# Performance work log

Hardware: AMD Instinct MI355X
Metric: run time of the kernel (lower is better)

The kernel has to match this reference:

```python
import jax, jax.numpy as jnp
import numpy as np

D = 1024
H = 16
DK = D // H  # 64
CHUNK = 64
EPS = 1e-5


def setup_inputs() -> dict:
    key = jax.random.key(0)
    k1, k2, k3 = jax.random.split(key, 3)
    x = jax.random.normal(k1, (4, 4096, D), dtype=jnp.float32)
    W_qkv = jax.random.normal(k2, (D, 3 * D), dtype=jnp.float32) * 0.02
    W_o = jax.random.normal(k3, (D, D), dtype=jnp.float32) * 0.02
    return {"x": x, "W_qkv": W_qkv, "W_o": W_o}


def _layernorm_noaffine(k):
    mu = jnp.mean(k, axis=-1, keepdims=True)
    var = jnp.mean((k - mu) ** 2, axis=-1, keepdims=True)  # biased var, torch LayerNorm
    return (k - mu) / jnp.sqrt(var + EPS)


def _linear_attn(x, W_qkv, W_o):
    B, L, Dm = x.shape
    qkv = (x @ W_qkv).reshape(B, L, 3, H, DK)
    q, k, v = qkv[:, :, 0], qkv[:, :, 1], qkv[:, :, 2]
    k = _layernorm_noaffine(k)

    nC = L // CHUNK
    # [nC, B, C, H, DK] for scan over chunks
    to_chunks = lambda t: t.reshape(B, nC, CHUNK, H, DK).transpose(1, 0, 2, 3, 4)
    qc, kc, vc = to_chunks(q), to_chunks(k), to_chunks(v)

    causal = jnp.tril(jnp.ones((CHUNK, CHUNK), dtype=bool))  # s <= t inclusive

    def step(S, chunk):
        q_c, k_c, v_c = chunk  # each [B, C, H, DK]
        # inter-chunk: y_t += S_prev @ q_t
        inter = jnp.einsum('bhde,bthe->bthd', S, q_c)
        # intra-chunk: y_t += sum_{s<=t} (k_s . q_t) v_s
        scores = jnp.einsum('bthd,bshd->bhts', q_c, k_c)
        scores = jnp.where(causal, scores, 0.0)
        intra = jnp.einsum('bhts,bshd->bthd', scores, v_c)
        # state update: S += sum_t v_t k_t^T
        S = S + jnp.einsum('bthd,bthe->bhde', v_c, k_c)
        return S, inter + intra

    S0 = jnp.zeros((B, H, DK, DK), dtype=x.dtype)
    _, ys = jax.lax.scan(step, S0, (qc, kc, vc))  # ys: [nC, B, C, H, DK]
    y = ys.transpose(1, 0, 2, 3, 4).reshape(B, L, Dm)
    return y @ W_o


def reference(x, W_qkv, W_o):
    return _linear_attn(x, W_qkv, W_o)
```

## Files before the change

kernel.cpp:

```cpp
#include <hip/hip_runtime.h>

#define EPS 1e-5f

typedef __attribute__((ext_vector_type(8))) short s16x8;
typedef __attribute__((ext_vector_type(4))) float f4;

__device__ __forceinline__ short f2bf(float f) {
  union { float f; unsigned u; } x; x.f = f;
  unsigned r = x.u + 0x7fffu + ((x.u >> 16) & 1u);
  return (short)(r >> 16);
}
__device__ __forceinline__ float bf2f(short s) {
  union { unsigned u; float f; } x; x.u = ((unsigned)(unsigned short)s) << 16;
  return x.f;
}
__device__ __forceinline__ void gll16(const short* g, short* l) {
  __builtin_amdgcn_global_load_lds((const __attribute__((address_space(1))) void*)g,
                                   (__attribute__((address_space(3))) void*)l, 16, 0, 0);
}

#define BAR() asm volatile("s_barrier" ::: "memory")
#define LGKM0() do { asm volatile("s_waitcnt lgkmcnt(0)" ::: "memory"); \
                     __builtin_amdgcn_sched_barrier(0); } while (0)

__global__ __launch_bounds__(256) void prep(
    const float* __restrict__ x, const float* __restrict__ Wqkv,
    const float* __restrict__ Wo,
    short* __restrict__ xb, short* __restrict__ WqkvT, short* __restrict__ WoT)
{
  __shared__ float tile[32][33];
  const int bid = blockIdx.x;
  if (bid < 8192) {
    const size_t i = ((size_t)bid * 256 + threadIdx.x) * 8;
    const float4* p = reinterpret_cast<const float4*>(x + i);
    float4 a = p[0], b = p[1];
    union { uint4 v; short s[8]; } o;
    o.s[0] = f2bf(a.x); o.s[1] = f2bf(a.y); o.s[2] = f2bf(a.z); o.s[3] = f2bf(a.w);
    o.s[4] = f2bf(b.x); o.s[5] = f2bf(b.y); o.s[6] = f2bf(b.z); o.s[7] = f2bf(b.w);
    *reinterpret_cast<uint4*>(xb + i) = o.v;
    return;
  }
  const float* W; short* WT; int K, N, t;
  if (bid < 11264) { W = Wqkv; WT = WqkvT; K = 1024; N = 3072; t = bid - 8192;  }
  else             { W = Wo;   WT = WoT;   K = 1024; N = 1024; t = bid - 11264; }
  const int nblk = N >> 5;
  const int n0 = (t % nblk) * 32, k0 = (t / nblk) * 32;
  const int tx = threadIdx.x & 31, ty = threadIdx.x >> 5;
  #pragma unroll
  for (int i = 0; i < 4; i++) {
    int r = ty + i * 8;
    tile[r][tx] = W[(size_t)(k0 + r) * N + n0 + tx];
  }
  __syncthreads();
  #pragma unroll
  for (int i = 0; i < 4; i++) {
    int r = ty + i * 8;
    WT[(size_t)(n0 + r) * K + k0 + tx] = f2bf(tile[tx][r]);
  }
}

__device__ __forceinline__ void stage_slice(const short* __restrict__ G, short* dstbase,
                                            int row0, int kcol, int rowgrp, int panel, int lane) {
  short* dst = dstbase + panel * 8192 + rowgrp * 512;
  const short* src = G + (size_t)(row0 + rowgrp * 16 + (lane >> 2)) * 1024
                       + kcol + panel * 32 + (((lane & 3) << 3) ^ ((lane >> 5) << 4));
  gll16(src, dst);
}

template<bool STAGE>
__device__ __forceinline__ void ktile8p(
    const short* ldsAc, const short* ldsBc, short* ldsAn, short* ldsBn,
    const short* __restrict__ A, const short* __restrict__ BT,
    int m0, int n0, int knext,
    int w, int lane, int wm, int wn, int quad, int l16,
    f4 (&acc)[8][4])
{
  s16x8 bfr[4][2];
  const int co = (quad << 3) ^ ((l16 >> 3) << 4);
  #pragma unroll
  for (int p = 0; p < 4; ++p) {
    s16x8 a00, a01, a10, a11;
    {
      const int r0 = (wm * 128 + p * 32 + l16) * 32;
      a00 = *reinterpret_cast<const s16x8*>(&ldsAc[r0 + co]);
      a01 = *reinterpret_cast<const s16x8*>(&ldsAc[8192 + r0 + co]);
      a10 = *reinterpret_cast<const s16x8*>(&ldsAc[r0 + 512 + co]);
      a11 = *reinterpret_cast<const s16x8*>(&ldsAc[8192 + r0 + 512 + co]);
    }
    if (p == 0) {
      #pragma unroll
      for (int nf = 0; nf < 4; ++nf) {
        const int rb = (wn * 64 + nf * 16 + l16) * 32;
        bfr[nf][0] = *reinterpret_cast<const s16x8*>(&ldsBc[rb + co]);
        bfr[nf][1] = *reinterpret_cast<const s16x8*>(&ldsBc[8192 + rb + co]);
      }
    }
    if (STAGE) {
      if (p == 0)      { stage_slice(BT, ldsBn, n0, knext, w,     0, lane); stage_slice(BT, ldsBn, n0, knext, w,     1, lane); }
      else if (p == 1) { stage_slice(BT, ldsBn, n0, knext, 8 + w, 0, lane); stage_slice(BT, ldsBn, n0, knext, 8 + w, 1, lane); }
      else if (p == 2) { const int rg = (w & 3) + ((w >> 2) << 3);
                         stage_slice(A, ldsAn, m0, knext, rg, 0, lane); stage_slice(A, ldsAn, m0, knext, rg, 1, lane); }
      else             { const int rg = 4 + (w & 3) + ((w >> 2) << 3);
                         stage_slice(A, ldsAn, m0, knext, rg, 0, lane); stage_slice(A, ldsAn, m0, knext, rg, 1, lane); }
    }
    BAR();
    LGKM0();
    __builtin_amdgcn_s_setprio(1);
    #pragma unroll
    for (int nf = 0; nf < 4; ++nf) {
      acc[2*p  ][nf] = __builtin_amdgcn_mfma_f32_16x16x32_bf16(a00, bfr[nf][0], acc[2*p  ][nf], 0, 0, 0);
      acc[2*p  ][nf] = __builtin_amdgcn_mfma_f32_16x16x32_bf16(a01, bfr[nf][1], acc[2*p  ][nf], 0, 0, 0);
      acc[2*p+1][nf] = __builtin_amdgcn_mfma_f32_16x16x32_bf16(a10, bfr[nf][0], acc[2*p+1][nf], 0, 0, 0);
      acc[2*p+1][nf] = __builtin_amdgcn_mfma_f32_16x16x32_bf16(a11, bfr[nf][1], acc[2*p+1][nf], 0, 0, 0);
    }
    __builtin_amdgcn_s_setprio(0);
    if (p == 1) {
      if (STAGE) asm volatile("s_waitcnt vmcnt(4)" ::: "memory");
      else       asm volatile("s_waitcnt vmcnt(0)" ::: "memory");
    }
    if (p == 3 && STAGE) asm volatile("s_waitcnt vmcnt(2)" ::: "memory");
    BAR();
  }
}

#define GEMM8P_PROLOGUE()                                                            \
  stage_slice(BT, Bb0, n0, 0, w,     0, lane); stage_slice(BT, Bb0, n0, 0, w,     1, lane); \
  stage_slice(BT, Bb0, n0, 0, 8 + w, 0, lane); stage_slice(BT, Bb0, n0, 0, 8 + w, 1, lane); \
  { const int rg = (w & 3) + ((w >> 2) << 3);                                        \
    stage_slice(A, Ab0, m0, 0, rg, 0, lane); stage_slice(A, Ab0, m0, 0, rg, 1, lane); } \
  { const int rg = 4 + (w & 3) + ((w >> 2) << 3);                                    \
    stage_slice(A, Ab0, m0, 0, rg, 0, lane); stage_slice(A, Ab0, m0, 0, rg, 1, lane); } \
  asm volatile("s_waitcnt vmcnt(2)" ::: "memory");                                   \
  BAR()

#define GEMM8P_MAINLOOP()                                                            \
  _Pragma("unroll 1")                                                                \
  for (int t = 0; t < 14; t += 2) {                                                  \
    ktile8p<true>(Ab0, Bb0, Ab1, Bb1, A, BT, m0, n0, (t + 1) << 6, w, lane, wm, wn, quad, l16, acc); \
    ktile8p<true>(Ab1, Bb1, Ab0, Bb0, A, BT, m0, n0, (t + 2) << 6, w, lane, wm, wn, quad, l16, acc); \
  }                                                                                  \
  ktile8p<true >(Ab0, Bb0, Ab1, Bb1, A, BT, m0, n0, 15 << 6, w, lane, wm, wn, quad, l16, acc); \
  ktile8p<false>(Ab1, Bb1, Ab0, Bb0, A, BT, m0, n0, 0,       w, lane, wm, wn, quad, l16, acc)

__global__ __launch_bounds__(512, 2) void gemm_qkv_8p(
    const short* __restrict__ A, const short* __restrict__ BT,
    short* __restrict__ qb, short* __restrict__ kb, short* __restrict__ vb)
{
  extern __shared__ __align__(16) short lds[];
  short* Ab0 = lds;           short* Ab1 = lds + 16384;
  short* Bb0 = lds + 32768;   short* Bb1 = lds + 49152;

  const int pid = blockIdx.x;
  const int wg = (pid & 7) * 96 + (pid >> 3);
  const int mb = wg / 12, nb = wg % 12;
  const int m0 = mb * 256, n0 = nb * 256;

  const int tid = threadIdx.x;
  const int w = tid >> 6, lane = tid & 63, quad = lane >> 4, l16 = lane & 15;
  const int wm = w >> 2, wn = w & 3;

  f4 acc[8][4];
  #pragma unroll
  for (int i = 0; i < 8; i++)
    #pragma unroll
    for (int j = 0; j < 4; j++) acc[i][j] = {0.f, 0.f, 0.f, 0.f};

  GEMM8P_PROLOGUE();
  GEMM8P_MAINLOOP();

  __syncthreads();
  short* st = lds + w * 1152;
  const int j0 = n0 + wn * 64;
  const int sq = j0 >> 10;
  const int hh = (j0 >> 6) & 15;
  short* dbuf = (sq == 0) ? qb : (sq == 1) ? kb : vb;
  const int r2 = lane >> 3, c8 = (lane & 7) << 3;
  #pragma unroll
  for (int mf = 0; mf < 8; ++mf) {
    #pragma unroll
    for (int nf = 0; nf < 4; ++nf)
      #pragma unroll
      for (int r = 0; r < 4; ++r)
        st[(quad * 4 + r) * 72 + nf * 16 + l16] = f2bf(acc[mf][nf][r]);
    #pragma unroll
    for (int h2 = 0; h2 < 2; ++h2) {
      int rr = h2 * 8 + r2;
      int i = m0 + wm * 128 + mf * 16 + rr;
      int bb = i >> 12, ll = i & 4095;
      uint4 val = *reinterpret_cast<const uint4*>(&st[rr * 72 + c8]);
      *reinterpret_cast<uint4*>(&dbuf[(((size_t)(bb * 16 + hh)) * 4096 + ll) * 64 + c8]) = val;
    }
  }
}

__global__ __launch_bounds__(512, 2) void gemm_out_8p(
    const short* __restrict__ A, const short* __restrict__ BT, float* __restrict__ C)
{
  extern __shared__ __align__(16) short lds[];
  short* Ab0 = lds;           short* Ab1 = lds + 16384;
  short* Bb0 = lds + 32768;   short* Bb1 = lds + 49152;

  const int pid = blockIdx.x;
  const int wg = (pid & 7) * 32 + (pid >> 3);
  const int mb = wg >> 2, nb = wg & 3;
  const int m0 = mb * 256, n0 = nb * 256;

  const int tid = threadIdx.x;
  const int w = tid >> 6, lane = tid & 63, quad = lane >> 4, l16 = lane & 15;
  const int wm = w >> 2, wn = w & 3;

  f4 acc[8][4];
  #pragma unroll
  for (int i = 0; i < 8; i++)
    #pragma unroll
    for (int j = 0; j < 4; j++) acc[i][j] = {0.f, 0.f, 0.f, 0.f};

  GEMM8P_PROLOGUE();
  GEMM8P_MAINLOOP();

  #pragma unroll
  for (int mf = 0; mf < 8; ++mf)
    #pragma unroll
    for (int nf = 0; nf < 4; ++nf)
      #pragma unroll
      for (int r = 0; r < 4; ++r) {
        int i = m0 + wm * 128 + mf * 16 + quad * 4 + r;
        int j = n0 + wn * 64 + nf * 16 + l16;
        C[(size_t)i * 1024 + j] = acc[mf][nf][r];
      }
}

__global__ __launch_bounds__(256) void gemm_qkv_v4(
    const short* __restrict__ A, const short* __restrict__ BT,
    short* __restrict__ qb, short* __restrict__ kb, short* __restrict__ vb)
{
  __shared__ __align__(16) short lds[8192];
  short* As = lds;
  short* Bs = lds + 4096;

  const int p = blockIdx.x;
  const int slot = p >> 3;
  const int strip = (p & 7) + 8 * (slot / 24);
  const int nb = slot % 24;
  const int m0 = strip * 128, n0 = nb * 128;

  const int tid = threadIdx.x;
  const int w = tid >> 6, lane = tid & 63, quad = lane >> 4, l16 = lane & 15;
  const int wm = (w >> 1) << 6, wn = (w & 1) << 6;

  f4 acc[4][4];
  #pragma unroll
  for (int i = 0; i < 4; i++)
    #pragma unroll
    for (int j = 0; j < 4; j++) acc[i][j] = {0.f, 0.f, 0.f, 0.f};

  const int row = w * 32 + (lane >> 2), ofs = (lane & 3) << 3;

  for (int k0 = 0; k0 < 1024; k0 += 32) {
    __syncthreads();
    gll16(A + (size_t)(m0 + row) * 1024 + k0 + ofs, &As[(w * 32) * 32]);
    gll16(A + (size_t)(m0 + row + 16) * 1024 + k0 + ofs, &As[(w * 32 + 16) * 32]);
    gll16(BT + (size_t)(n0 + row) * 1024 + k0 + ofs, &Bs[(w * 32) * 32]);
    gll16(BT + (size_t)(n0 + row + 16) * 1024 + k0 + ofs, &Bs[(w * 32 + 16) * 32]);
    __syncthreads();
    s16x8 afr[4], bfr[4];
    #pragma unroll
    for (int t = 0; t < 4; t++)
      afr[t] = *reinterpret_cast<const s16x8*>(&As[(wm + t * 16 + l16) * 32 + quad * 8]);
    #pragma unroll
    for (int t = 0; t < 4; t++)
      bfr[t] = *reinterpret_cast<const s16x8*>(&Bs[(wn + t * 16 + l16) * 32 + quad * 8]);
    #pragma unroll
    for (int ti = 0; ti < 4; ti++)
      #pragma unroll
      for (int tj = 0; tj < 4; tj++)
        acc[ti][tj] = __builtin_amdgcn_mfma_f32_16x16x32_bf16(afr[ti], bfr[tj], acc[ti][tj], 0, 0, 0);
  }

  __syncthreads();
  short* st = &lds[w * 16 * 72];
  const int j0 = n0 + wn;
  const int sq = j0 >> 10;
  const int hh = (j0 >> 6) & 15;
  short* dbuf = (sq == 0) ? qb : (sq == 1) ? kb : vb;
  const int r2 = lane >> 3, c8 = (lane & 7) << 3;
  #pragma unroll
  for (int ti = 0; ti < 4; ti++) {
    #pragma unroll
    for (int tj = 0; tj < 4; tj++)
      #pragma unroll
      for (int r = 0; r < 4; r++)
        st[(quad * 4 + r) * 72 + tj * 16 + l16] = f2bf(acc[ti][tj][r]);
    #pragma unroll
    for (int h2 = 0; h2 < 2; h2++) {
      int rr = h2 * 8 + r2;
      int i = m0 + wm + ti * 16 + rr;
      int bb = i >> 12, ll = i & 4095;
      uint4 val = *reinterpret_cast<const uint4*>(&st[rr * 72 + c8]);
      *reinterpret_cast<uint4*>(&dbuf[(((size_t)(bb * 16 + hh)) * 4096 + ll) * 64 + c8]) = val;
    }
  }
}

__global__ __launch_bounds__(256) void ln_k(short* __restrict__ kbuf)
{
  const int row = blockIdx.x * 4 + (threadIdx.x >> 6);
  const int lane = threadIdx.x & 63;
  const size_t idx = (size_t)row * 64 + lane;
  float v = bf2f(kbuf[idx]);
  float s = v, s2 = v * v;
  #pragma unroll
  for (int off = 32; off; off >>= 1) {
    s += __shfl_xor(s, off);
    s2 += __shfl_xor(s2, off);
  }
  float mean = s * (1.f / 64.f);
  float var = s2 * (1.f / 64.f) - mean * mean;
  float rstd = rsqrtf(var + EPS);
  kbuf[idx] = f2bf((v - mean) * rstd);
}

__global__ __launch_bounds__(256) void macro_outer(
    const short* __restrict__ kb, const short* __restrict__ vb,
    short* __restrict__ G)
{
  __shared__ __align__(16) short kT[64 * 72];
  __shared__ __align__(16) short vT[64 * 72];
  const int bh = blockIdx.x >> 4, mc = blockIdx.x & 15;
  const int tid = threadIdx.x;
  const int w = tid >> 6, lane = tid & 63, quad = lane >> 4, l16 = lane & 15;
  const int srow = tid >> 2, sseg = (tid & 3) << 4;
  const int toff = ((((srow >> 3) ^ ((tid & 3) << 1)) & 7) << 3) + (srow & 7);
  const int gsw = (w & 3) << 1;

  f4 accG[4];
  #pragma unroll
  for (int tj = 0; tj < 4; tj++) accG[tj] = {0.f, 0.f, 0.f, 0.f};

  for (int j = 0; j < 4; ++j) {
    if (j) __syncthreads();
    const size_t base = (size_t)bh * 262144 + (size_t)((mc * 4 + j) * 64 + srow) * 64 + sseg;
    {
      const float4* kp = reinterpret_cast<const float4*>(kb + base);
      union { float4 v[2]; short s[16]; } ku;
      ku.v[0] = kp[0]; ku.v[1] = kp[1];
      float kv[16]; float s = 0.f, s2 = 0.f;
      #pragma unroll
      for (int i = 0; i < 16; i++) { kv[i] = bf2f(ku.s[i]); s += kv[i]; s2 += kv[i] * kv[i]; }
      s += __shfl_xor(s, 1);  s2 += __shfl_xor(s2, 1);
      s += __shfl_xor(s, 2);  s2 += __shfl_xor(s2, 2);
      float mean = s * (1.f / 64.f);
      float var = s2 * (1.f / 64.f) - mean * mean;
      float rstd = rsqrtf(var + EPS);
      #pragma unroll
      for (int i = 0; i < 16; i++) kT[(sseg + i) * 72 + toff] = f2bf((kv[i] - mean) * rstd);
      const float4* vp = reinterpret_cast<const float4*>(vb + base);
      union { float4 v[2]; short s[16]; } vu;
      vu.v[0] = vp[0]; vu.v[1] = vp[1];
      #pragma unroll
      for (int i = 0; i < 16; i++) vT[(sseg + i) * 72 + toff] = vu.s[i];
    }
    __syncthreads();
    s16x8 va0 = *reinterpret_cast<const s16x8*>(&vT[(w * 16 + l16) * 72 + ((quad ^ gsw) << 3)]);
    s16x8 va1 = *reinterpret_cast<const s16x8*>(&vT[(w * 16 + l16) * 72 + (((4 + quad) ^ gsw) << 3)]);
    #pragma unroll
    for (int tj = 0; tj < 4; tj++) {
      const int gk = tj << 1;
      s16x8 kb0 = *reinterpret_cast<const s16x8*>(&kT[(tj * 16 + l16) * 72 + ((quad ^ gk) << 3)]);
      s16x8 kb1 = *reinterpret_cast<const s16x8*>(&kT[(tj * 16 + l16) * 72 + (((4 + quad) ^ gk) << 3)]);
      accG[tj] = __builtin_amdgcn_mfma_f32_16x16x32_bf16(va0, kb0, accG[tj], 0, 0, 0);
      accG[tj] = __builtin_amdgcn_mfma_f32_16x16x32_bf16(va1, kb1, accG[tj], 0, 0, 0);
    }
  }
  short* Gc = G + (size_t)blockIdx.x * 4096;
  #pragma unroll
  for (int tj = 0; tj < 4; tj++)
    #pragma unroll
    for (int r = 0; r < 4; r++)
      Gc[(w * 16 + quad * 4 + r) * 64 + tj * 16 + l16] = f2bf(accG[tj][r]);
}

__global__ __launch_bounds__(128) void prefix_S16(short* __restrict__ G)
{
  const int bh = blockIdx.x >> 3, rg = blockIdx.x & 7;
  short* p = G + (size_t)bh * 65536 + rg * 512 + threadIdx.x * 4;
  float s0 = 0.f, s1 = 0.f, s2 = 0.f, s3 = 0.f;
  union U { uint2 v; short s[4]; };
  U cur; cur.v = *reinterpret_cast<const uint2*>(p);
  #pragma unroll 4
  for (int mc = 0; mc < 16; mc++) {
    short* pc = p + (size_t)mc * 4096;
    U nxt; nxt.v = cur.v;
    if (mc < 15) nxt.v = *reinterpret_cast<const uint2*>(pc + 4096);
    float g0 = bf2f(cur.s[0]), g1 = bf2f(cur.s[1]), g2 = bf2f(cur.s[2]), g3 = bf2f(cur.s[3]);
    U su;
    su.s[0] = f2bf(s0); su.s[1] = f2bf(s1); su.s[2] = f2bf(s2); su.s[3] = f2bf(s3);
    *reinterpret_cast<uint2*>(pc) = su.v;
    s0 += g0; s1 += g1; s2 += g2; s3 += g3;
    cur = nxt;
  }
}

__global__ __launch_bounds__(256) void macro_out(
    const short* __restrict__ qb, const short* __restrict__ kb,
    const short* __restrict__ vb, const short* __restrict__ G,
    short* __restrict__ yb)
{
  __shared__ __align__(16) short ks[64 * 72];
  __shared__ __align__(16) short kT[64 * 72];
  __shared__ __align__(16) short vT[64 * 72];
  __shared__ __align__(16) short Sb[64 * 72];
  __shared__ __align__(16) short Ps[64 * 72];
  const int bh = blockIdx.x >> 4, mc = blockIdx.x & 15;
  const int b = bh >> 4, h = bh & 15;
  const int tid = threadIdx.x;
  const int w = tid >> 6, lane = tid & 63, quad = lane >> 4, l16 = lane & 15;
  const int srow = tid >> 2, sseg = (tid & 3) << 4;
  const int toff = ((((srow >> 3) ^ ((tid & 3) << 1)) & 7) << 3) + (srow & 7);
  const int gsw = (w & 3) << 1;
  const int rq2 = ((l16 >> 2) & 3) << 1;

  const short* Sg = G + (size_t)blockIdx.x * 4096;
  f4 accS[4];
  #pragma unroll
  for (int tj = 0; tj < 4; tj++)
    #pragma unroll
    for (int r = 0; r < 4; r++)
      accS[tj][r] = bf2f(Sg[(w * 16 + quad * 4 + r) * 64 + tj * 16 + l16]);

  for (int j = 0; j < 4; ++j) {
    const int c = mc * 4 + j;
    if (j) __syncthreads();
    #pragma unroll
    for (int tj = 0; tj < 4; tj++) {
      const int eb = (tj << 1) + (l16 >> 3);
      const int sbc = (((eb ^ (quad << 1)) & 7) << 3) + (l16 & 7);
      #pragma unroll
      for (int r = 0; r < 4; r++)
        Sb[(w * 16 + quad * 4 + r) * 72 + sbc] = f2bf(accS[tj][r]);
    }
    const size_t base = (size_t)bh * 262144 + (size_t)(c * 64 + srow) * 64 + sseg;
    {
      const float4* kp = reinterpret_cast<const float4*>(kb + base);
      union { float4 v[2]; short s[16]; } ku;
      ku.v[0] = kp[0]; ku.v[1] = kp[1];
      float kv[16]; float s = 0.f, s2 = 0.f;
      #pragma unroll
      for (int i = 0; i < 16; i++) { kv[i] = bf2f(ku.s[i]); s += kv[i]; s2 += kv[i] * kv[i]; }
      s += __shfl_xor(s, 1);  s2 += __shfl_xor(s2, 1);
      s += __shfl_xor(s, 2);  s2 += __shfl_xor(s2, 2);
      float mean = s * (1.f / 64.f);
      float var = s2 * (1.f / 64.f) - mean * mean;
      float rstd = rsqrtf(var + EPS);
      union { float4 v[2]; short s[16]; } ko;
      #pragma unroll
      for (int i = 0; i < 16; i++) ko.s[i] = f2bf((kv[i] - mean) * rstd);
      *reinterpret_cast<float4*>(&ks[srow * 72 + sseg]) = ko.v[0];
      *reinterpret_cast<float4*>(&ks[srow * 72 + sseg + 8]) = ko.v[1];
      #pragma unroll
      for (int i = 0; i < 16; i++) kT[(sseg + i) * 72 + toff] = ko.s[i];
      const float4* vp = reinterpret_cast<const float4*>(vb + base);
      union { float4 v[2]; short s[16]; } vu;
      vu.v[0] = vp[0]; vu.v[1] = vp[1];
      #pragma unroll
      for (int i = 0; i < 16; i++) vT[(sseg + i) * 72 + toff] = vu.s[i];
    }
    s16x8 qa[4][2];
    const size_t qbase = (size_t)bh * 262144 + (size_t)c * 4096;
    #pragma unroll
    for (int ti = 0; ti < 4; ti++)
      #pragma unroll
      for (int kh = 0; kh < 2; kh++)
        qa[ti][kh] = *reinterpret_cast<const s16x8*>(
            qb + qbase + (size_t)(ti * 16 + l16) * 64 + kh * 32 + quad * 8);
    __syncthreads();
    s16x8 kf[2], sf[2];
    #pragma unroll
    for (int kh = 0; kh < 2; kh++) {
      kf[kh] = *reinterpret_cast<const s16x8*>(&ks[(w * 16 + l16) * 72 + kh * 32 + quad * 8]);
      sf[kh] = *reinterpret_cast<const s16x8*>(&Sb[(w * 16 + l16) * 72 + ((((kh << 2) + quad) ^ rq2) << 3)]);
    }
    const int psoff = (((((w * 16 + l16) >> 3) ^ (quad << 1)) & 7) << 3) + (l16 & 7);
    #pragma unroll
    for (int ti = 0; ti < 4; ti++) {
      f4 z = {0.f, 0.f, 0.f, 0.f};
      z = __builtin_amdgcn_mfma_f32_16x16x32_bf16(qa[ti][0], kf[0], z, 0, 0, 0);
      z = __builtin_amdgcn_mfma_f32_16x16x32_bf16(qa[ti][1], kf[1], z, 0, 0, 0);
      #pragma unroll
      for (int r = 0; r < 4; r++) {
        int t = ti * 16 + quad * 4 + r;
        int s = w * 16 + l16;
        Ps[t * 72 + psoff] = (s <= t) ? f2bf(z[r]) : (short)0;
      }
    }
    __syncthreads();
    s16x8 vf0 = *reinterpret_cast<const s16x8*>(&vT[(w * 16 + l16) * 72 + ((quad ^ gsw) << 3)]);
    s16x8 vf1 = *reinterpret_cast<const s16x8*>(&vT[(w * 16 + l16) * 72 + (((4 + quad) ^ gsw) << 3)]);
    #pragma unroll
    for (int ti = 0; ti < 4; ti++) {
      f4 z = {0.f, 0.f, 0.f, 0.f};
      s16x8 p0 = *reinterpret_cast<const s16x8*>(&Ps[(ti * 16 + l16) * 72 + ((quad ^ rq2) << 3)]);
      s16x8 p1 = *reinterpret_cast<const s16x8*>(&Ps[(ti * 16 + l16) * 72 + (((4 + quad) ^ rq2) << 3)]);
      z = __builtin_amdgcn_mfma_f32_16x16x32_bf16(p0, vf0, z, 0, 0, 0);
      z = __builtin_amdgcn_mfma_f32_16x16x32_bf16(p1, vf1, z, 0, 0, 0);
      z = __builtin_amdgcn_mfma_f32_16x16x32_bf16(qa[ti][0], sf[0], z, 0, 0, 0);
      z = __builtin_amdgcn_mfma_f32_16x16x32_bf16(qa[ti][1], sf[1], z, 0, 0, 0);
      #pragma unroll
      for (int r = 0; r < 4; r++) {
        int t = ti * 16 + quad * 4 + r;
        int d = w * 16 + l16;
        yb[(((size_t)b * 4096) + c * 64 + t) * 1024 + h * 64 + d] = f2bf(z[r]);
      }
    }
    #pragma unroll
    for (int tj = 0; tj < 4; tj++) {
      const int gk = tj << 1;
      s16x8 ub0 = *reinterpret_cast<const s16x8*>(&kT[(tj * 16 + l16) * 72 + ((quad ^ gk) << 3)]);
      s16x8 ub1 = *reinterpret_cast<const s16x8*>(&kT[(tj * 16 + l16) * 72 + (((4 + quad) ^ gk) << 3)]);
      accS[tj] = __builtin_amdgcn_mfma_f32_16x16x32_bf16(vf0, ub0, accS[tj], 0, 0, 0);
      accS[tj] = __builtin_amdgcn_mfma_f32_16x16x32_bf16(vf1, ub1, accS[tj], 0, 0, 0);
    }
  }
}

__global__ __launch_bounds__(256) void gemm_out_v3(
    const short* __restrict__ A, const short* __restrict__ BT, float* __restrict__ C)
{
  __shared__ __align__(16) short As[128 * 32];
  __shared__ __align__(16) short Bs[128 * 32];
  const int p = blockIdx.x;
  const int slot = p >> 3;
  const int strip = (p & 7) + 8 * (slot >> 3);
  const int nb = slot & 7;
  const int m0 = strip * 128, n0 = nb * 128;
  const int tid = threadIdx.x;
  const int w = tid >> 6, lane = tid & 63, quad = lane >> 4, l16 = lane & 15;
  const int wm = (w >> 1) << 6, wn = (w & 1) << 6;

  f4 acc[4][4];
  #pragma unroll
  for (int i = 0; i < 4; i++)
    #pragma unroll
    for (int j = 0; j < 4; j++) acc[i][j] = {0.f, 0.f, 0.f, 0.f};

  const int row = w * 32 + (lane >> 2), ofs = (lane & 3) << 3;

  for (int k0 = 0; k0 < 1024; k0 += 32) {
    __syncthreads();
    gll16(A + (size_t)(m0 + row) * 1024 + k0 + ofs, &As[(w * 32) * 32]);
    gll16(A + (size_t)(m0 + row + 16) * 1024 + k0 + ofs, &As[(w * 32 + 16) * 32]);
    gll16(BT + (size_t)(n0 + row) * 1024 + k0 + ofs, &Bs[(w * 32) * 32]);
    gll16(BT + (size_t)(n0 + row + 16) * 1024 + k0 + ofs, &Bs[(w * 32 + 16) * 32]);
    __syncthreads();
    s16x8 afr[4], bfr[4];
    #pragma unroll
    for (int t = 0; t < 4; t++)
      afr[t] = *reinterpret_cast<const s16x8*>(&As[(wm + t * 16 + l16) * 32 + quad * 8]);
    #pragma unroll
    for (int t = 0; t < 4; t++)
      bfr[t] = *reinterpret_cast<const s16x8*>(&Bs[(wn + t * 16 + l16) * 32 + quad * 8]);
    #pragma unroll
    for (int ti = 0; ti < 4; ti++)
      #pragma unroll
      for (int tj = 0; tj < 4; tj++)
        acc[ti][tj] = __builtin_amdgcn_mfma_f32_16x16x32_bf16(afr[ti], bfr[tj], acc[ti][tj], 0, 0, 0);
  }
  #pragma unroll
  for (int ti = 0; ti < 4; ti++)
    #pragma unroll
    for (int tj = 0; tj < 4; tj++)
      #pragma unroll
      for (int r = 0; r < 4; r++) {
        int i = m0 + wm + ti * 16 + quad * 4 + r;
        int j = n0 + wn + tj * 16 + l16;
        C[(size_t)i * 1024 + j] = acc[ti][tj][r];
      }
}

__global__ __launch_bounds__(256) void gemm_qkv_r1(
    const float* __restrict__ A, const float* __restrict__ B,
    short* __restrict__ qb, short* __restrict__ kb, short* __restrict__ vb)
{
  __shared__ __align__(16) short As[128 * 40];
  __shared__ __align__(16) short Bs[128 * 40];
  const int n0 = blockIdx.x * 128;
  const int m0 = blockIdx.y * 128;
  const int tid = threadIdx.x;
  const int w = tid >> 6, lane = tid & 63, quad = lane >> 4, l16 = lane & 15;
  const int wm = (w >> 1) << 6, wn = (w & 1) << 6;
  f4 acc[4][4];
  #pragma unroll
  for (int i = 0; i < 4; i++)
    #pragma unroll
    for (int j = 0; j < 4; j++) acc[i][j] = {0.f, 0.f, 0.f, 0.f};
  const int arow = tid >> 1, aseg = (tid & 1) << 4;
  const int brow = tid >> 3, bseg = (tid & 7) << 4;
  for (int k0 = 0; k0 < 1024; k0 += 32) {
    __syncthreads();
    {
      const float4* ap = reinterpret_cast<const float4*>(A + (size_t)(m0 + arow) * 1024 + k0 + aseg);
      union { float4 v[4]; float f[16]; } af;
      af.v[0] = ap[0]; af.v[1] = ap[1]; af.v[2] = ap[2]; af.v[3] = ap[3];
      union { float4 v[2]; short s[16]; } ao;
      #pragma unroll
      for (int i = 0; i < 16; i++) ao.s[i] = f2bf(af.f[i]);
      float4* dst = reinterpret_cast<float4*>(&As[arow * 40 + aseg]);
      dst[0] = ao.v[0]; dst[1] = ao.v[1];
    }
    {
      const float4* bp = reinterpret_cast<const float4*>(B + (size_t)(k0 + brow) * 3072 + n0 + bseg);
      union { float4 v[4]; float f[16]; } bu;
      bu.v[0] = bp[0]; bu.v[1] = bp[1]; bu.v[2] = bp[2]; bu.v[3] = bp[3];
      #pragma unroll
      for (int i = 0; i < 16; i++) Bs[(bseg + i) * 40 + brow] = f2bf(bu.f[i]);
    }
    __syncthreads();
    s16x8 afr[4], bfr[4];
    #pragma unroll
    for (int t = 0; t < 4; t++)
      afr[t] = *reinterpret_cast<const s16x8*>(&As[(wm + t * 16 + l16) * 40 + quad * 8]);
    #pragma unroll
    for (int t = 0; t < 4; t++)
      bfr[t] = *reinterpret_cast<const s16x8*>(&Bs[(wn + t * 16 + l16) * 40 + quad * 8]);
    #pragma unroll
    for (int ti = 0; ti < 4; ti++)
      #pragma unroll
      for (int tj = 0; tj < 4; tj++)
        acc[ti][tj] = __builtin_amdgcn_mfma_f32_16x16x32_bf16(afr[ti], bfr[tj], acc[ti][tj], 0, 0, 0);
  }
  const int sq = n0 >> 10;
  short* dbuf = (sq == 0) ? qb : (sq == 1) ? kb : vb;
  #pragma unroll
  for (int ti = 0; ti < 4; ti++)
    #pragma unroll
    for (int tj = 0; tj < 4; tj++)
      #pragma unroll
      for (int r = 0; r < 4; r++) {
        int i = m0 + wm + ti * 16 + quad * 4 + r;
        int j = n0 + wn + tj * 16 + l16;
        int hh = (j >> 6) & 15, dd = j & 63;
        int bb = i >> 12, ll = i & 4095;
        dbuf[(((size_t)(bb * 16 + hh)) * 4096 + ll) * 64 + dd] = f2bf(acc[ti][tj][r]);
      }
}

__global__ __launch_bounds__(256) void scan_chunks_r1(
    const short* __restrict__ qb, const short* __restrict__ kb,
    const short* __restrict__ vb, short* __restrict__ yb)
{
  __shared__ __align__(16) short qs[64 * 72];
  __shared__ __align__(16) short ks[64 * 72];
  __shared__ __align__(16) short kT[64 * 72];
  __shared__ __align__(16) short vT[64 * 72];
  __shared__ __align__(16) short Sb[64 * 72];
  __shared__ __align__(16) short Ps[64 * 72];
  const int bh = blockIdx.x;
  const int b = bh >> 4, h = bh & 15;
  const int tid = threadIdx.x;
  const int w = tid >> 6, lane = tid & 63, quad = lane >> 4, l16 = lane & 15;
  const int srow = tid >> 2, sseg = (tid & 3) << 4;
  const size_t base = (size_t)bh * 4096 * 64;
  f4 accS[4];
  #pragma unroll
  for (int i = 0; i < 4; i++) accS[i] = {0.f, 0.f, 0.f, 0.f};
  for (int c = 0; c < 64; c++) {
    __syncthreads();
    {
      size_t g = base + ((size_t)(c * 64 + srow)) * 64 + sseg;
      const float4* qp = reinterpret_cast<const float4*>(qb + g);
      float4 q0 = qp[0], q1 = qp[1];
      *reinterpret_cast<float4*>(&qs[srow * 72 + sseg]) = q0;
      *reinterpret_cast<float4*>(&qs[srow * 72 + sseg + 8]) = q1;
      const float4* kp = reinterpret_cast<const float4*>(kb + g);
      union { float4 v[2]; short s[16]; } ku;
      ku.v[0] = kp[0]; ku.v[1] = kp[1];
      *reinterpret_cast<float4*>(&ks[srow * 72 + sseg]) = ku.v[0];
      *reinterpret_cast<float4*>(&ks[srow * 72 + sseg + 8]) = ku.v[1];
      #pragma unroll
      for (int i = 0; i < 16; i++) kT[(sseg + i) * 72 + srow] = ku.s[i];
      const float4* vp = reinterpret_cast<const float4*>(vb + g);
      union { float4 v[2]; short s[16]; } vu;
      vu.v[0] = vp[0]; vu.v[1] = vp[1];
      #pragma unroll
      for (int i = 0; i < 16; i++) vT[(sseg + i) * 72 + srow] = vu.s[i];
    }
    #pragma unroll
    for (int ti = 0; ti < 4; ti++)
      #pragma unroll
      for (int r = 0; r < 4; r++)
        Sb[(ti * 16 + quad * 4 + r) * 72 + w * 16 + l16] = f2bf(accS[ti][r]);
    __syncthreads();
    s16x8 qa[4][2];
    #pragma unroll
    for (int ti = 0; ti < 4; ti++)
      #pragma unroll
      for (int kh = 0; kh < 2; kh++)
        qa[ti][kh] = *reinterpret_cast<const s16x8*>(&qs[(ti * 16 + l16) * 72 + kh * 32 + quad * 8]);
    s16x8 kf[2];
    #pragma unroll
    for (int kh = 0; kh < 2; kh++)
      kf[kh] = *reinterpret_cast<const s16x8*>(&ks[(w * 16 + l16) * 72 + kh * 32 + quad * 8]);
    #pragma unroll
    for (int ti = 0; ti < 4; ti++) {
      f4 z = {0.f, 0.f, 0.f, 0.f};
      z = __builtin_amdgcn_mfma_f32_16x16x32_bf16(qa[ti][0], kf[0], z, 0, 0, 0);
      z = __builtin_amdgcn_mfma_f32_16x16x32_bf16(qa[ti][1], kf[1], z, 0, 0, 0);
      #pragma unroll
      for (int r = 0; r < 4; r++) {
        int t = ti * 16 + quad * 4 + r;
        int s = w * 16 + l16;
        Ps[t * 72 + s] = (s <= t) ? f2bf(z[r]) : (short)0;
      }
    }
    __syncthreads();
    s16x8 vf[2], sf[2];
    #pragma unroll
    for (int kh = 0; kh < 2; kh++) {
      vf[kh] = *reinterpret_cast<const s16x8*>(&vT[(w * 16 + l16) * 72 + kh * 32 + quad * 8]);
      sf[kh] = *reinterpret_cast<const s16x8*>(&Sb[(w * 16 + l16) * 72 + kh * 32 + quad * 8]);
    }
    #pragma unroll
    for (int ti = 0; ti < 4; ti++) {
      f4 z = {0.f, 0.f, 0.f, 0.f};
      s16x8 p0 = *reinterpret_cast<const s16x8*>(&Ps[(ti * 16 + l16) * 72 + quad * 8]);
      s16x8 p1 = *reinterpret_cast<const s16x8*>(&Ps[(ti * 16 + l16) * 72 + 32 + quad * 8]);
      z = __builtin_amdgcn_mfma_f32_16x16x32_bf16(p0, vf[0], z, 0, 0, 0);
      z = __builtin_amdgcn_mfma_f32_16x16x32_bf16(p1, vf[1], z, 0, 0, 0);
      z = __builtin_amdgcn_mfma_f32_16x16x32_bf16(qa[ti][0], sf[0], z, 0, 0, 0);
      z = __builtin_amdgcn_mfma_f32_16x16x32_bf16(qa[ti][1], sf[1], z, 0, 0, 0);
      #pragma unroll
      for (int r = 0; r < 4; r++) {
        int t = ti * 16 + quad * 4 + r;
        int d = w * 16 + l16;
        yb[(((size_t)b * 4096) + c * 64 + t) * 1024 + h * 64 + d] = f2bf(z[r]);
      }
    }
    s16x8 ku0 = *reinterpret_cast<const s16x8*>(&kT[(w * 16 + l16) * 72 + quad * 8]);
    s16x8 ku1 = *reinterpret_cast<const s16x8*>(&kT[(w * 16 + l16) * 72 + 32 + quad * 8]);
    #pragma unroll
    for (int ti = 0; ti < 4; ti++) {
      s16x8 va0 = *reinterpret_cast<const s16x8*>(&vT[(ti * 16 + l16) * 72 + quad * 8]);
      s16x8 va1 = *reinterpret_cast<const s16x8*>(&vT[(ti * 16 + l16) * 72 + 32 + quad * 8]);
      accS[ti] = __builtin_amdgcn_mfma_f32_16x16x32_bf16(va0, ku0, accS[ti], 0, 0, 0);
      accS[ti] = __builtin_amdgcn_mfma_f32_16x16x32_bf16(va1, ku1, accS[ti], 0, 0, 0);
    }
  }
}

__global__ __launch_bounds__(256) void gemm_out_r1(
    const short* __restrict__ A, const float* __restrict__ B, float* __restrict__ C)
{
  __shared__ __align__(16) short As[128 * 40];
  __shared__ __align__(16) short Bs[128 * 40];
  const int n0 = blockIdx.x * 128;
  const int m0 = blockIdx.y * 128;
  const int tid = threadIdx.x;
  const int w = tid >> 6, lane = tid & 63, quad = lane >> 4, l16 = lane & 15;
  const int wm = (w >> 1) << 6, wn = (w & 1) << 6;
  f4 acc[4][4];
  #pragma unroll
  for (int i = 0; i < 4; i++)
    #pragma unroll
    for (int j = 0; j < 4; j++) acc[i][j] = {0.f, 0.f, 0.f, 0.f};
  const int arow = tid >> 1, aseg = (tid & 1) << 4;
  const int brow = tid >> 3, bseg = (tid & 7) << 4;
  for (int k0 = 0; k0 < 1024; k0 += 32) {
    __syncthreads();
    {
      const float4* ap = reinterpret_cast<const float4*>(A + (size_t)(m0 + arow) * 1024 + k0 + aseg);
      float4 a0 = ap[0], a1 = ap[1];
      float4* dst = reinterpret_cast<float4*>(&As[arow * 40 + aseg]);
      dst[0] = a0; dst[1] = a1;
    }
    {
      const float4* bp = reinterpret_cast<const float4*>(B + (size_t)(k0 + brow) * 1024 + n0 + bseg);
      union { float4 v[4]; float f[16]; } bu;
      bu.v[0] = bp[0]; bu.v[1] = bp[1]; bu.v[2] = bp[2]; bu.v[3] = bp[3];
      #pragma unroll
      for (int i = 0; i < 16; i++) Bs[(bseg + i) * 40 + brow] = f2bf(bu.f[i]);
    }
    __syncthreads();
    s16x8 afr[4], bfr[4];
    #pragma unroll
    for (int t = 0; t < 4; t++)
      afr[t] = *reinterpret_cast<const s16x8*>(&As[(wm + t * 16 + l16) * 40 + quad * 8]);
    #pragma unroll
    for (int t = 0; t < 4; t++)
      bfr[t] = *reinterpret_cast<const s16x8*>(&Bs[(wn + t * 16 + l16) * 40 + quad * 8]);
    #pragma unroll
    for (int ti = 0; ti < 4; ti++)
      #pragma unroll
      for (int tj = 0; tj < 4; tj++)
        acc[ti][tj] = __builtin_amdgcn_mfma_f32_16x16x32_bf16(afr[ti], bfr[tj], acc[ti][tj], 0, 0, 0);
  }
  #pragma unroll
  for (int ti = 0; ti < 4; ti++)
    #pragma unroll
    for (int tj = 0; tj < 4; tj++)
      #pragma unroll
      for (int r = 0; r < 4; r++) {
        int i = m0 + wm + ti * 16 + quad * 4 + r;
        int j = n0 + wn + tj * 16 + l16;
        C[(size_t)i * 1024 + j] = acc[ti][tj][r];
      }
}

extern "C" void kernel_launch(void* const* d_in, const int* in_sizes, int n_in,
                              void* d_out, int out_size, void* d_ws, size_t ws_size,
                              hipStream_t stream) {
  const float* x    = (const float*)d_in[0];
  const float* Wqkv = (const float*)d_in[1];
  const float* Wo   = (const float*)d_in[2];
  float* out = (float*)d_out;

  short* qb = (short*)d_ws;
  short* kb = qb + (size_t)16777216;
  short* vb = kb + (size_t)16777216;
  short* yb = vb + (size_t)16777216;

  const size_t NEED = 176160768;
  if (ws_size >= NEED) {
    short* Gs    = yb + (size_t)16777216;
    short* WqkvT = Gs + (size_t)16777216;
    short* WoT   = WqkvT + (size_t)3145728;
    short* xb    = Gs;

    static int use8p = -1;
    if (use8p < 0) {
      hipError_t e1 = hipFuncSetAttribute((const void*)gemm_qkv_8p,
          hipFuncAttributeMaxDynamicSharedMemorySize, 131072);
      hipError_t e2 = hipFuncSetAttribute((const void*)gemm_out_8p,
          hipFuncAttributeMaxDynamicSharedMemorySize, 131072);
      use8p = (e1 == hipSuccess && e2 == hipSuccess) ? 1 : 0;
    }

    prep          <<<dim3(12288),   256, 0, stream>>>(x, Wqkv, Wo, xb, WqkvT, WoT);
    if (use8p)
      gemm_qkv_8p <<<dim3(768),     512, 131072, stream>>>(xb, WqkvT, qb, kb, vb);
    else
      gemm_qkv_v4 <<<dim3(3072),    256, 0, stream>>>(xb, WqkvT, qb, kb, vb);
    macro_outer   <<<dim3(1024),    256, 0, stream>>>(kb, vb, Gs);
    prefix_S16    <<<dim3(512),     128, 0, stream>>>(Gs);
    macro_out     <<<dim3(1024),    256, 0, stream>>>(qb, kb, vb, Gs, yb);
    if (use8p)
      gemm_out_8p <<<dim3(256),     512, 131072, stream>>>(yb, WoT, out);
    else
      gemm_out_v3 <<<dim3(1024),    256, 0, stream>>>(yb, WoT, out);
  } else {
    gemm_qkv_r1   <<<dim3(24, 128), 256, 0, stream>>>(x, Wqkv, qb, kb, vb);
    ln_k          <<<dim3(65536),   256, 0, stream>>>(kb);
    scan_chunks_r1<<<dim3(64),      256, 0, stream>>>(qb, kb, vb, yb);
    gemm_out_r1   <<<dim3(8, 128),  256, 0, stream>>>(yb, Wo, out);
  }
}
```

Measured before the change: 302.9 us.

## Fold prefix-sum into macro_out, prefetch K/V chunks, stage y through LDS

Removes the separate prefix_S16 launch. Each macro_out block now sums the preceding chunk-group states from G itself, accumulating in fp32 rather than reading a bf16 prefix. Both macro kernels register-prefetch the next chunk's K and V rows while the current chunk is processed, to hide global load latency. The y output is staged through LDS so it can be written with coalesced 16-byte stores instead of scattered 2-byte stores. In exchange, later blocks read up to 15 extra G tiles and each chunk iteration gets one more barrier.

```diff
diff --git a/kernel.cpp b/kernel.cpp
--- a/kernel.cpp
+++ b/kernel.cpp
@@ -337,16 +337,23 @@
   #pragma unroll
   for (int tj = 0; tj < 4; tj++) accG[tj] = {0.f, 0.f, 0.f, 0.f};
 
+  union F4x2 { float4 v[2]; short s[16]; };
+  F4x2 kcur, vcur;
+  {
+    const size_t b0 = (size_t)bh * 262144 + (size_t)((mc * 4) * 64 + srow) * 64 + sseg;
+    const float4* kp = reinterpret_cast<const float4*>(kb + b0);
+    const float4* vp = reinterpret_cast<const float4*>(vb + b0);
+    kcur.v[0] = kp[0]; kcur.v[1] = kp[1];
+    vcur.v[0] = vp[0]; vcur.v[1] = vp[1];
+  }
+
+  #pragma unroll
   for (int j = 0; j < 4; ++j) {
     if (j) __syncthreads();
-    const size_t base = (size_t)bh * 262144 + (size_t)((mc * 4 + j) * 64 + srow) * 64 + sseg;
     {
-      const float4* kp = reinterpret_cast<const float4*>(kb + base);
-      union { float4 v[2]; short s[16]; } ku;
-      ku.v[0] = kp[0]; ku.v[1] = kp[1];
       float kv[16]; float s = 0.f, s2 = 0.f;
       #pragma unroll
-      for (int i = 0; i < 16; i++) { kv[i] = bf2f(ku.s[i]); s += kv[i]; s2 += kv[i] * kv[i]; }
+      for (int i = 0; i < 16; i++) { kv[i] = bf2f(kcur.s[i]); s += kv[i]; s2 += kv[i] * kv[i]; }
       s += __shfl_xor(s, 1);  s2 += __shfl_xor(s2, 1);
       s += __shfl_xor(s, 2);  s2 += __shfl_xor(s2, 2);
       float mean = s * (1.f / 64.f);
@@ -354,11 +361,16 @@
       float rstd = rsqrtf(var + EPS);
       #pragma unroll
       for (int i = 0; i < 16; i++) kT[(sseg + i) * 72 + toff] = f2bf((kv[i] - mean) * rstd);
-      const float4* vp = reinterpret_cast<const float4*>(vb + base);
-      union { float4 v[2]; short s[16]; } vu;
-      vu.v[0] = vp[0]; vu.v[1] = vp[1];
-      #pragma unroll
-      for (int i = 0; i < 16; i++) vT[(sseg + i) * 72 + toff] = vu.s[i];
+      #pragma unroll
+      for (int i = 0; i < 16; i++) vT[(sseg + i) * 72 + toff] = vcur.s[i];
+    }
+    F4x2 knxt, vnxt;
+    if (j < 3) {
+      const size_t bn = (size_t)bh * 262144 + (size_t)((mc * 4 + j + 1) * 64 + srow) * 64 + sseg;
+      const float4* kp = reinterpret_cast<const float4*>(kb + bn);
+      const float4* vp = reinterpret_cast<const float4*>(vb + bn);
+      knxt.v[0] = kp[0]; knxt.v[1] = kp[1];
+      vnxt.v[0] = vp[0]; vnxt.v[1] = vp[1];
     }
     __syncthreads();
     s16x8 va0 = *reinterpret_cast<const s16x8*>(&vT[(w * 16 + l16) * 72 + ((quad ^ gsw) << 3)]);
@@ -371,6 +383,7 @@
       accG[tj] = __builtin_amdgcn_mfma_f32_16x16x32_bf16(va0, kb0, accG[tj], 0, 0, 0);
       accG[tj] = __builtin_amdgcn_mfma_f32_16x16x32_bf16(va1, kb1, accG[tj], 0, 0, 0);
     }
+    if (j < 3) { kcur = knxt; vcur = vnxt; }
   }
   short* Gc = G + (size_t)blockIdx.x * 4096;
   #pragma unroll
@@ -378,27 +391,6 @@
     #pragma unroll
     for (int r = 0; r < 4; r++)
       Gc[(w * 16 + quad * 4 + r) * 64 + tj * 16 + l16] = f2bf(accG[tj][r]);
-}
-
-__global__ __launch_bounds__(128) void prefix_S16(short* __restrict__ G)
-{
-  const int bh = blockIdx.x >> 3, rg = blockIdx.x & 7;
-  short* p = G + (size_t)bh * 65536 + rg * 512 + threadIdx.x * 4;
-  float s0 = 0.f, s1 = 0.f, s2 = 0.f, s3 = 0.f;
-  union U { uint2 v; short s[4]; };
-  U cur; cur.v = *reinterpret_cast<const uint2*>(p);
-  #pragma unroll 4
-  for (int mc = 0; mc < 16; mc++) {
-    short* pc = p + (size_t)mc * 4096;
-    U nxt; nxt.v = cur.v;
-    if (mc < 15) nxt.v = *reinterpret_cast<const uint2*>(pc + 4096);
-    float g0 = bf2f(cur.s[0]), g1 = bf2f(cur.s[1]), g2 = bf2f(cur.s[2]), g3 = bf2f(cur.s[3]);
-    U su;
-    su.s[0] = f2bf(s0); su.s[1] = f2bf(s1); su.s[2] = f2bf(s2); su.s[3] = f2bf(s3);
-    *reinterpret_cast<uint2*>(pc) = su.v;
-    s0 += g0; s1 += g1; s2 += g2; s3 += g3;
-    cur = nxt;
-  }
 }
 
 __global__ __launch_bounds__(256) void macro_out(
@@ -420,14 +412,29 @@
   const int gsw = (w & 3) << 1;
   const int rq2 = ((l16 >> 2) & 3) << 1;
 
-  const short* Sg = G + (size_t)blockIdx.x * 4096;
   f4 accS[4];
   #pragma unroll
-  for (int tj = 0; tj < 4; tj++)
-    #pragma unroll
-    for (int r = 0; r < 4; r++)
-      accS[tj][r] = bf2f(Sg[(w * 16 + quad * 4 + r) * 64 + tj * 16 + l16]);
-
+  for (int tj = 0; tj < 4; tj++) accS[tj] = {0.f, 0.f, 0.f, 0.f};
+  for (int m = 0; m < mc; ++m) {
+    const short* Sg = G + ((size_t)(bh * 16 + m)) * 4096;
+    #pragma unroll
+    for (int tj = 0; tj < 4; tj++)
+      #pragma unroll
+      for (int r = 0; r < 4; r++)
+        accS[tj][r] += bf2f(Sg[(w * 16 + quad * 4 + r) * 64 + tj * 16 + l16]);
+  }
+
+  union F4x2 { float4 v[2]; short s[16]; };
+  F4x2 kcur, vcur;
+  {
+    const size_t b0 = (size_t)bh * 262144 + (size_t)((mc * 4) * 64 + srow) * 64 + sseg;
+    const float4* kp = reinterpret_cast<const float4*>(kb + b0);
+    const float4* vp = reinterpret_cast<const float4*>(vb + b0);
+    kcur.v[0] = kp[0]; kcur.v[1] = kp[1];
+    vcur.v[0] = vp[0]; vcur.v[1] = vp[1];
+  }
+
+  #pragma unroll
   for (int j = 0; j < 4; ++j) {
     const int c = mc * 4 + j;
     if (j) __syncthreads();
@@ -439,40 +446,41 @@
       for (int r = 0; r < 4; r++)
         Sb[(w * 16 + quad * 4 + r) * 72 + sbc] = f2bf(accS[tj][r]);
     }
-    const size_t base = (size_t)bh * 262144 + (size_t)(c * 64 + srow) * 64 + sseg;
+    s16x8 qa[4][2];
+    const size_t qbase = (size_t)bh * 262144 + (size_t)c * 4096;
+    #pragma unroll
+    for (int ti = 0; ti < 4; ti++)
+      #pragma unroll
+      for (int kh = 0; kh < 2; kh++)
+        qa[ti][kh] = *reinterpret_cast<const s16x8*>(
+            qb + qbase + (size_t)(ti * 16 + l16) * 64 + kh * 32 + quad * 8);
     {
-      const float4* kp = reinterpret_cast<const float4*>(kb + base);
-      union { float4 v[2]; short s[16]; } ku;
-      ku.v[0] = kp[0]; ku.v[1] = kp[1];
       float kv[16]; float s = 0.f, s2 = 0.f;
       #pragma unroll
-      for (int i = 0; i < 16; i++) { kv[i] = bf2f(ku.s[i]); s += kv[i]; s2 += kv[i] * kv[i]; }
+      for (int i = 0; i < 16; i++) { kv[i] = bf2f(kcur.s[i]); s += kv[i]; s2 += kv[i] * kv[i]; }
       s += __shfl_xor(s, 1);  s2 += __shfl_xor(s2, 1);
       s += __shfl_xor(s, 2);  s2 += __shfl_xor(s2, 2);
       float mean = s * (1.f / 64.f);
       float var = s2 * (1.f / 64.f) - mean * mean;
       float rstd = rsqrtf(var + EPS);
-      union { float4 v[2]; short s[16]; } ko;
+      F4x2 ko;
       #pragma unroll
       for (int i = 0; i < 16; i++) ko.s[i] = f2bf((kv[i] - mean) * rstd);
       *reinterpret_cast<float4*>(&ks[srow * 72 + sseg]) = ko.v[0];
       *reinterpret_cast<float4*>(&ks[srow * 72 + sseg + 8]) = ko.v[1];
       #pragma unroll
       for (int i = 0; i < 16; i++) kT[(sseg + i) * 72 + toff] = ko.s[i];
-      const float4* vp = reinterpret_cast<const float4*>(vb + base);
-      union { float4 v[2]; short s[16]; } vu;
-      vu.v[0] = vp[0]; vu.v[1] = vp[1];
-      #pragma unroll
-      for (int i = 0; i < 16; i++) vT[(sseg + i) * 72 + toff] = vu.s[i];
-    }
-    s16x8 qa[4][2];
-    const size_t qbase = (size_t)bh * 262144 + (size_t)c * 4096;
-    #pragma unroll
-    for (int ti = 0; ti < 4; ti++)
-      #pragma unroll
-      for (int kh = 0; kh < 2; kh++)
-        qa[ti][kh] = *reinterpret_cast<const s16x8*>(
-            qb + qbase + (size_t)(ti * 16 + l16) * 64 + kh * 32 + quad * 8);
+      #pragma unroll
+      for (int i = 0; i < 16; i++) vT[(sseg + i) * 72 + toff] = vcur.s[i];
+    }
+    F4x2 knxt, vnxt;
+    if (j < 3) {
+      const size_t bn = (size_t)bh * 262144 + (size_t)((c + 1) * 64 + srow) * 64 + sseg;
+      const float4* kp = reinterpret_cast<const float4*>(kb + bn);
+      const float4* vp = reinterpret_cast<const float4*>(vb + bn);
+      knxt.v[0] = kp[0]; knxt.v[1] = kp[1];
+      vnxt.v[0] = vp[0]; vnxt.v[1] = vp[1];
+    }
     __syncthreads();
     s16x8 kf[2], sf[2];
     #pragma unroll
@@ -506,11 +514,8 @@
       z = __builtin_amdgcn_mfma_f32_16x16x32_bf16(qa[ti][0], sf[0], z, 0, 0, 0);
       z = __builtin_amdgcn_mfma_f32_16x16x32_bf16(qa[ti][1], sf[1], z, 0, 0, 0);
       #pragma unroll
-      for (int r = 0; r < 4; r++) {
-        int t = ti * 16 + quad * 4 + r;
-        int d = w * 16 + l16;
-        yb[(((size_t)b * 4096) + c * 64 + t) * 1024 + h * 64 + d] = f2bf(z[r]);
-      }
+      for (int r = 0; r < 4; r++)
+        ks[(ti * 16 + quad * 4 + r) * 72 + w * 16 + l16] = f2bf(z[r]);
     }
     #pragma unroll
     for (int tj = 0; tj < 4; tj++) {
@@ -520,6 +525,16 @@
       accS[tj] = __builtin_amdgcn_mfma_f32_16x16x32_bf16(vf0, ub0, accS[tj], 0, 0, 0);
       accS[tj] = __builtin_amdgcn_mfma_f32_16x16x32_bf16(vf1, ub1, accS[tj], 0, 0, 0);
     }
+    __syncthreads();
+    {
+      const int r = tid >> 2, sg = (tid & 3) << 4;
+      const uint4* src = reinterpret_cast<const uint4*>(&ks[r * 72 + sg]);
+      uint4 v0 = src[0], v1 = src[1];
+      uint4* dst = reinterpret_cast<uint4*>(
+          &yb[(((size_t)b * 4096) + c * 64 + r) * 1024 + h * 64 + sg]);
+      dst[0] = v0; dst[1] = v1;
+    }
+    if (j < 3) { kcur = knxt; vcur = vnxt; }
   }
 }
 
@@ -840,7 +855,6 @@
     else
       gemm_qkv_v4 <<<dim3(3072),    256, 0, stream>>>(xb, WqkvT, qb, kb, vb);
     macro_outer   <<<dim3(1024),    256, 0, stream>>>(kb, vb, Gs);
-    prefix_S16    <<<dim3(512),     128, 0, stream>>>(Gs);
     macro_out     <<<dim3(1024),    256, 0, stream>>>(qb, kb, vb, Gs, yb);
     if (use8p)
       gemm_out_8p <<<dim3(256),     512, 131072, stream>>>(yb, WoT, out);
```

New measurement: 306.0 us. About the same (+1.0%).
